# Performance work log

Hardware: AMD Instinct MI355X
Metric: run time of the kernel (lower is better)

Reference implementation:

```python
import jax, jax.numpy as jnp
import numpy as np
from jax import lax

MAX_C = 16       # MAX_MERGE_NUMS
COND_THRES = 0.2
IOU_THRES = 0.3
CLASS_OFFSET = 1e4  # shift per-class so cross-class BEV IoU == 0 (emulates per-class loop)


def setup_inputs() -> dict:
    key = jax.random.key(0)
    k1, k2, k3, k4, k5 = jax.random.split(key, 5)
    B, N = 4, 4096
    # realistic 3D boxes: centers, positive sizes, heading
    centers = jax.random.normal(k1, (B, N, 3), jnp.float32) * 20.0
    sizes = jax.random.uniform(k2, (B, N, 3), jnp.float32, 0.5, 4.5)
    heading = jax.random.uniform(k3, (B, N, 1), jnp.float32, -np.pi, np.pi)
    boxes = jnp.concatenate([centers, sizes, heading], -1)  # [B,N,7]
    scores = jax.random.uniform(k4, (B, N), jnp.float32)
    labels = jax.random.randint(k5, (B, N), 0, 3, jnp.int32)
    kw = jax.random.split(jax.random.fold_in(key, 1), 2)
    W1 = jax.random.normal(kw[0], (7, 64), jnp.float32) * 0.3
    b1 = jnp.zeros((64,), jnp.float32)
    W2 = jax.random.normal(kw[1], (64, 1), jnp.float32) * 0.3
    b2 = jnp.zeros((1,), jnp.float32)
    return {"boxes": boxes, "scores": scores, "labels": labels,
            "W1": W1, "b1": b1, "W2": W2, "b2": b2}


def _nms_merge_frame(boxes, scores, labels, W1, b1, W2, b2):
    # boxes [N,7], scores [N], labels [N] int32
    N = boxes.shape[0]
    valid = scores > COND_THRES                       # cond_mask
    skey = jnp.where(valid, scores, -jnp.inf)
    order = jnp.argsort(-skey)                        # score descending
    boxes, scores = boxes[order], scores[order]
    labels, valid = labels[order], valid[order]

    # nearest-BEV (axis-aligned) IoU; class offset keeps classes disjoint
    off = labels.astype(boxes.dtype) * CLASS_OFFSET
    cx, cy = boxes[:, 0] + off, boxes[:, 1]
    hx, hy = boxes[:, 3] * 0.5, boxes[:, 4] * 0.5
    x1, x2, y1, y2 = cx - hx, cx + hx, cy - hy, cy + hy
    ix = jnp.clip(jnp.minimum(x2[:, None], x2[None]) - jnp.maximum(x1[:, None], x1[None]), 0.0)
    iy = jnp.clip(jnp.minimum(y2[:, None], y2[None]) - jnp.maximum(y1[:, None], y1[None]), 0.0)
    inter = ix * iy                                   # [N,N]
    area = (x2 - x1) * (y2 - y1)
    iou = inter / jnp.clip(area[:, None] + area[None] - inter, 1e-6)
    overlap = iou > IOU_THRES                         # includes self

    # greedy clustering: highest-score remaining box leads its cluster
    def body(i, st):
        alive, cid = st
        lead = alive[i]
        take = alive & overlap[i] & lead
        cid = jnp.where(take, i, cid)
        return alive & (~take), cid
    alive, cid = lax.fori_loop(0, N, body,
                               (valid, jnp.full((N,), -1, jnp.int32)))
    leader = cid == jnp.arange(N, dtype=jnp.int32)    # cluster representatives

    # rank of each box within its cluster (score order preserved)
    idx = jnp.arange(N)
    same = (cid[None, :] == cid[:, None]) & (cid[:, None] >= 0)
    rank = (same & (idx[None, :] < idx[:, None])).sum(-1)  # [N]

    # scatter up to MAX_C members per cluster (zero-padded buffers)
    dest = jnp.where((cid >= 0) & (rank < MAX_C), cid, N)  # N = dump row
    clusters = jnp.zeros((N + 1, MAX_C, 7), boxes.dtype)
    clusters = clusters.at[dest, jnp.minimum(rank, MAX_C - 1)].set(boxes)[:N]

    # merge network: per-box MLP -> softmax weights over cluster slots
    h = jax.nn.relu(clusters @ W1 + b1)               # [N,MAX_C,64]
    logits = (h @ W2 + b2)[..., 0]                    # [N,MAX_C]
    slot_ok = jnp.any(clusters != 0, -1)
    logits = jnp.where(slot_ok, logits, -1e9)
    w = jax.nn.softmax(logits, -1)
    merged = jnp.einsum('nc,ncd->nd', w, clusters)    # [N,7]

    # masked scatter: non-positive merged sizes fall back to leader sizes
    size = jnp.where(merged[:, 3:6] <= 0, boxes[:, 3:6], merged[:, 3:6])
    out_box = jnp.concatenate([merged[:, :3], size, merged[:, 6:7]], -1)
    info = jnp.concatenate([out_box, scores[:, None],
                            labels.astype(boxes.dtype)[:, None]], -1)  # [N,9]
    info = jnp.where(leader[:, None], info, 0.0)
    return info, leader


def reference(boxes, scores, labels, W1, b1, W2, b2):
    info, leader = jax.vmap(_nms_merge_frame,
                            in_axes=(0, 0, 0, None, None, None, None))(
        boxes, scores, labels, W1, b1, W2, b2)
    return info, leader
```

## Files before the change

kernel.cpp:

```cpp
#include <hip/hip_runtime.h>
#include <stdint.h>

#pragma clang fp contract(off)

#define BF 4
#define NN 4096
#define MAXC 16
#define PL 2048
#define WL 32
#define WF 24
#define TRI_CAP (64 * (WL * (WL + 1) / 2))

typedef unsigned long long u64;
typedef uint32_t u32;

__device__ __forceinline__ u64 shfl64(u64 v, int src) {
  return (u64)__shfl((long long)v, src, 64);
}
__device__ __forceinline__ u64 readlane64(u64 v, int l) {
  u32 lo = (u32)__builtin_amdgcn_readlane((int)(u32)v, l);
  u32 hi = (u32)__builtin_amdgcn_readlane((int)(u32)(v >> 32), l);
  return ((u64)hi << 32) | lo;
}
__device__ __forceinline__ u64 greedy64_iso(u64 D, u64 rem, u64 onlyme) {
  u64 lead = 0;
  while (rem) {
    u64 t = D & rem;
    u64 iso = __ballot(t == onlyme) & rem;
    lead |= iso;
    rem &= ~iso;
    if (!rem) break;
    int b = __builtin_ctzll(rem);
    lead |= 1ull << b;
    rem &= ~readlane64(D, b);
    if (!rem) break;
    b = __builtin_ctzll(rem);
    lead |= 1ull << b;
    rem &= ~readlane64(D, b);
  }
  return lead;
}

__global__ __launch_bounds__(1024) void sort_kernel(
    const float* __restrict__ scores, u64* __restrict__ keyS)
{
  __shared__ u64 keyA[NN];
  __shared__ u64 keyB[NN];
  __shared__ int cnt16[16][65];
  __shared__ int waveTot[16];
  __shared__ int waveBase[16];
  const int f = blockIdx.x, tid = threadIdx.x;
  const int wave = tid >> 6, lane = tid & 63;
  const u64 ltmask = (1ull << lane) - 1ull;

  for (int s = 0; s < 4; s++) {
    int idx = tid + 1024 * s;
    float sc = scores[f * NN + idx];
    bool valid = sc > 0.2f;
    u32 bits = __float_as_uint(sc);
    u32 m = bits ^ ((bits >> 31) ? 0xFFFFFFFFu : 0x80000000u);
    u32 hi = valid ? ~m : 0xFFFFFFFFu;
    keyA[idx] = ((u64)hi << 32) | (u32)idx;
  }
  __syncthreads();

  u64* src = keyA;
  u64* dst = keyB;
  for (int pass = 0; pass < 7; pass++) {
    const int shift = 32 + 4 * pass;
    u64 kreg[4]; int dreg[4], rreg[4];
    for (int s = 0; s < 4; s++) {
      const int c = wave * 4 + s;
      u64 k = src[c * 64 + lane];
      int d = (int)((k >> shift) & 15);
      u64 B0 = __ballot((d & 1) != 0);
      u64 B1 = __ballot((d & 2) != 0);
      u64 B2 = __ballot((d & 4) != 0);
      u64 B3 = __ballot((d & 8) != 0);
      u64 M = ((d & 1) ? B0 : ~B0) & ((d & 2) ? B1 : ~B1)
            & ((d & 4) ? B2 : ~B2) & ((d & 8) ? B3 : ~B3);
      rreg[s] = __popcll(M & ltmask);
      int bin = lane & 15;
      u64 Mb = ((bin & 1) ? B0 : ~B0) & ((bin & 2) ? B1 : ~B1)
             & ((bin & 4) ? B2 : ~B2) & ((bin & 8) ? B3 : ~B3);
      if (lane < 16) cnt16[bin][c] = __popcll(Mb);
      kreg[s] = k; dreg[s] = d;
    }
    __syncthreads();
    {
      int v = cnt16[wave][lane];
      int incl = v;
      for (int off2 = 1; off2 < 64; off2 <<= 1) {
        int up = __shfl_up(incl, off2, 64);
        if (lane >= off2) incl += up;
      }
      if (lane == 63) waveTot[wave] = incl;
      __syncthreads();
      if (wave == 0) {
        int tv = (lane < 16) ? waveTot[lane] : 0;
        int ts = tv;
        for (int off2 = 1; off2 < 16; off2 <<= 1) {
          int up = __shfl_up(ts, off2, 64);
          if (lane >= off2) ts += up;
        }
        if (lane < 16) waveBase[lane] = ts - tv;
      }
      __syncthreads();
      cnt16[wave][lane] = waveBase[wave] + incl - v;
    }
    __syncthreads();
    for (int s = 0; s < 4; s++) {
      const int c = wave * 4 + s;
      int pos = cnt16[dreg[s]][c] + rreg[s];
      dst[pos] = kreg[s];
    }
    __syncthreads();
    u64* tmp = src; src = dst; dst = tmp;
  }
  for (int s = 0; s < 4; s++) {
    int p = tid + 1024 * s;
    keyS[f * NN + p] = src[p];
  }
}

__global__ __launch_bounds__(256) void countscan_kernel(
    const u64* __restrict__ keyS, const int* __restrict__ labels,
    int* __restrict__ chunkOffG, int* __restrict__ VbufL)
{
  __shared__ int cnt[64][3];
  const int f = blockIdx.x, tid = threadIdx.x;
  const int wave = tid >> 6, lane = tid & 63;
  for (int s = 0; s < 16; s++) {
    int chunk = wave * 16 + s;
    int p = chunk * 64 + lane;
    u64 kv = keyS[f * NN + p];
    bool valid = (u32)(kv >> 32) != 0xFFFFFFFFu;
    int g = (int)(kv & 0xFFFFFFFFull);
    int l = valid ? labels[f * NN + g] : 3;
    u64 B0 = __ballot((l & 1) != 0);
    u64 B1 = __ballot((l & 2) != 0);
    if (lane < 3) {
      u64 Mb = ((lane & 1) ? B0 : ~B0) & ((lane & 2) ? B1 : ~B1);
      cnt[chunk][lane] = __popcll(Mb);
    }
  }
  __syncthreads();
  if (wave == 0) {
    for (int ll = 0; ll < 3; ll++) {
      int v = cnt[lane][ll];
      int incl = v;
      for (int off2 = 1; off2 < 64; off2 <<= 1) {
        int up = __shfl_up(incl, off2, 64);
        if (lane >= off2) incl += up;
      }
      chunkOffG[(f * 64 + lane) * 3 + ll] = incl - v;
      if (lane == 63) VbufL[f * 3 + ll] = incl;
    }
  }
}

__global__ __launch_bounds__(256) void gather_kernel(
    const u64* __restrict__ keyS, const float* __restrict__ boxes,
    const float* __restrict__ scores, const int* __restrict__ labels,
    const int* __restrict__ chunkOffG,
    float* __restrict__ sboxes, float* __restrict__ sscore, float* __restrict__ slabel,
    int* __restrict__ lab_slot, int* __restrict__ loc_slot,
    int* __restrict__ pglob,
    float* __restrict__ px1, float* __restrict__ px2, float* __restrict__ py1,
    float* __restrict__ py2, float* __restrict__ parea)
{
  const int gs = blockIdx.x * 256 + threadIdx.x;
  const int f = gs >> 12, p = gs & (NN - 1);
  const int lane = threadIdx.x & 63, chunk = p >> 6;
  const u64 ltmask = (1ull << lane) - 1ull;
  u64 kv = keyS[gs];
  bool valid = (u32)(kv >> 32) != 0xFFFFFFFFu;
  int g = (int)(kv & 0xFFFFFFFFull);
  const float* bp = boxes + (size_t)(f * NN + g) * 7;
  float b0 = bp[0], b1v = bp[1], b2v = bp[2], b3 = bp[3], b4 = bp[4], b5 = bp[5], b6 = bp[6];
  int lab = labels[f * NN + g];
  const int o = f * NN + p;
  float* sb = sboxes + (size_t)o * 7;
  sb[0] = b0; sb[1] = b1v; sb[2] = b2v; sb[3] = b3; sb[4] = b4; sb[5] = b5; sb[6] = b6;
  sscore[o] = scores[f * NN + g];
  slabel[o] = (float)lab;
  int l = valid ? lab : 3;
  u64 B0 = __ballot((l & 1) != 0);
  u64 B1 = __ballot((l & 2) != 0);
  u64 M = ((l & 1) ? B0 : ~B0) & ((l & 2) ? B1 : ~B1);
  int rank = __popcll(M & ltmask);
  if (l < 3) {
    int loc = chunkOffG[(f * 64 + chunk) * 3 + l] + rank;
    int pi = (f * 3 + l) * PL + loc;
    float off = (float)l * 10000.0f;
    float cx = b0 + off, cy = b1v;
    float hx = b3 * 0.5f, hy = b4 * 0.5f;
    float x1 = cx - hx, x2 = cx + hx, y1 = cy - hy, y2 = cy + hy;
    float area = (x2 - x1) * (y2 - y1);
    pglob[pi] = p;
    px1[pi] = x1; px2[pi] = x2; py1[pi] = y1; py2[pi] = y2; parea[pi] = area;
    lab_slot[o] = l; loc_slot[o] = loc;
  } else {
    lab_slot[o] = -1; loc_slot[o] = -1;
  }
}

__global__ __launch_bounds__(256) void mask_kernel(
    const float* __restrict__ px1, const float* __restrict__ px2,
    const float* __restrict__ py1, const float* __restrict__ py2,
    const float* __restrict__ parea, const int* __restrict__ pglob,
    const int* __restrict__ VbufL,
    u64* __restrict__ maskP, u64* __restrict__ triT)
{
  __shared__ float4 cbox[1024];
  __shared__ float carea[1024];
  const int bx = blockIdx.x;
  const int fl = bx >> 8, rem = bx & 255;
  const int rt = rem >> 1, wt = rem & 1;
  const int r0 = rt * 16;
  const int Vl = VbufL[fl];
  if (r0 >= Vl) return;
  if (wt * 1024 >= Vl) return;
  const int tid = threadIdx.x;
  for (int q = tid; q < 1024; q += 256) {
    int c = fl * PL + wt * 1024 + q;
    cbox[q] = make_float4(px1[c], px2[c], py1[c], py2[c]);
    carea[q] = parea[c];
  }
  __syncthreads();
  const int row = r0 + (tid & 15);
  const int wl = tid >> 4;
  const int cw = wt * 16 + wl;
  const int nc = Vl - cw * 64;
  if (row >= Vl || nc <= 0) return;
  const int rg = fl * PL + row;
  const float rx1 = px1[rg], rx2 = px2[rg], ry1 = py1[rg], ry2 = py2[rg], ra = parea[rg];
  u64 bits = 0;
  const int qb = wl * 64;
  for (int b = 0; b < 64; b++) {
    float4 cb = cbox[qb + b];
    float ca = carea[qb + b];
    float ix = fminf(rx2, cb.y) - fmaxf(rx1, cb.x);
    ix = fmaxf(ix, 0.0f);
    float iy = fminf(ry2, cb.w) - fmaxf(ry1, cb.z);
    iy = fmaxf(iy, 0.0f);
    float inter = ix * iy;
    float den = fmaxf((ra + ca) - inter, 1e-6f);
    float iou = inter / den;
    bits |= ((u64)(iou > 0.3f)) << b;
  }
  if (nc < 64) bits &= (1ull << nc) - 1ull;
  const int f = fl / 3;
  const int p = pglob[fl * PL + row];
  maskP[((size_t)f * NN + p) * WL + cw] = bits;
  if (row >= 64 * cw) {
    const int W = (Vl + 63) >> 6;
    int base = 64 * (cw * W - (cw * (cw - 1)) / 2);
    triT[(size_t)fl * TRI_CAP + base + (row - 64 * cw)] = bits;
  }
}

__global__ __launch_bounds__(64) void nms_kernel(
    const u64* __restrict__ triT, const int* __restrict__ VbufL,
    u64* __restrict__ leadersP)
{
  __shared__ u64 tri[64 * (WF * (WF + 1) / 2) + 128];
  const int fl = blockIdx.x, lane = threadIdx.x;
  const int Vl = VbufL[fl];
  const int W = (Vl + 63) >> 6;
  const u64* mT = triT + (size_t)fl * TRI_CAP;
  const u64 onlyme = 1ull << lane;
  u64 alive = 0;
  if (lane < WL) {
    int rb = Vl - 64 * lane;
    alive = (rb >= 64) ? ~0ull : ((rb > 0) ? ((1ull << rb) - 1ull) : 0ull);
  }
  u64 myLead = 0;

  if (W > 0 && W <= WF) {
    const int totw = 64 * (W * (W + 1) / 2);
    const int nch = (totw * 8 + 1023) >> 10;
    const char* g = (const char*)mT;
    char* l = (char*)tri;
    int batch = 0;
    for (int it = 0; it < nch; it++) {
      __builtin_amdgcn_global_load_lds(
          (const __attribute__((address_space(1))) unsigned int*)(g + (size_t)it * 1024 + (size_t)lane * 16),
          (__attribute__((address_space(3))) unsigned int*)(l + (size_t)it * 1024),
          16, 0, 0);
      if (++batch == 48) {
        asm volatile("s_waitcnt vmcnt(0)" ::: "memory");
        batch = 0;
      }
    }
    asm volatile("s_waitcnt vmcnt(0)" ::: "memory");
    int offw = 0;
    u64 D = tri[lane];
    for (int w = 0; w < W; w++) {
      const int offw_next = offw + 64 * (W - w);
      u64 Dnext = (w + 1 < W) ? tri[offw_next + lane] : 0;
      u64 lead = greedy64_iso(D, readlane64(alive, w), onlyme);
      if (lane == w) myLead = lead;
      if (lead) {
        const u64* strm = tri + offw;
        int v = w + 1;
        for (; v + 3 < W; v += 4) {
          u64 a0 = strm[64 * (v - w) + lane];
          u64 a1 = strm[64 * (v + 1 - w) + lane];
          u64 a2 = strm[64 * (v + 2 - w) + lane];
          u64 a3 = strm[64 * (v + 3 - w) + lane];
          u64 c0 = __ballot((a0 & lead) != 0ull);
          u64 c1 = __ballot((a1 & lead) != 0ull);
          u64 c2 = __ballot((a2 & lead) != 0ull);
          u64 c3 = __ballot((a3 & lead) != 0ull);
          if (lane == v)     alive &= ~c0;
          if (lane == v + 1) alive &= ~c1;
          if (lane == v + 2) alive &= ~c2;
          if (lane == v + 3) alive &= ~c3;
        }
        for (; v < W; v++) {
          u64 a0 = strm[64 * (v - w) + lane];
          u64 c0 = __ballot((a0 & lead) != 0ull);
          if (lane == v) alive &= ~c0;
        }
      }
      D = Dnext;
      offw = offw_next;
    }
  } else if (W > 0) {
    int offw = 0;
    for (int w = 0; w < W; w++) {
      const u64* strm = mT + offw;
      u64 D = strm[lane];
      u64 lead = greedy64_iso(D, readlane64(alive, w), onlyme);
      if (lane == w) myLead = lead;
      if (lead) {
        for (int v = w + 1; v < W; v++) {
          u64 a0 = strm[64 * (v - w) + lane];
          u64 c0 = __ballot((a0 & lead) != 0ull);
          if (lane == v) alive &= ~c0;
        }
      }
      offw += 64 * (W - w);
    }
  }
  if (lane < WL) leadersP[fl * WL + lane] = myLead;
}

__global__ __launch_bounds__(256) void cid_kernel(
    const u64* __restrict__ maskP, const u64* __restrict__ leadersP,
    const int* __restrict__ lab_slot, const int* __restrict__ loc_slot,
    const int* __restrict__ VbufL, int* __restrict__ cidP)
{
  const int g = blockIdx.x * 4 + (threadIdx.x >> 6);
  const int lane = threadIdx.x & 63;
  const int f = g >> 12, p = g & (NN - 1);
  const int l = lab_slot[f * NN + p];
  if (l < 0) return;
  const int fl = f * 3 + l;
  const int loc = loc_slot[f * NN + p];
  const int Wl = (VbufL[fl] + 63) >> 6;
  u64 L = 0, m = 0;
  if (lane < Wl) {
    L = leadersP[fl * WL + lane];
    m = maskP[((size_t)f * NN + p) * WL + lane];
  }
  const int g6 = loc >> 6, b6 = loc & 63;
  u64 pmask = (lane < g6) ? ~0ull
            : (lane == g6 ? ((b6 == 63) ? ~0ull : ((1ull << (b6 + 1)) - 1ull)) : 0ull);
  u64 v = m & L & pmask;
  u64 bl = __ballot(v != 0ull);
  int cid = -1;
  if (bl != 0ull) {
    int w = __builtin_ctzll(bl);
    u64 vw = shfl64(v, w);
    cid = w * 64 + __builtin_ctzll(vw);
  }
  if (lane == 0) cidP[fl * PL + loc] = cid;
}

__global__ __launch_bounds__(64) void mm_kernel(
    const u64* __restrict__ maskP, const u64* __restrict__ leadersP,
    const int* __restrict__ cidP, const int* __restrict__ lab_slot,
    const int* __restrict__ loc_slot, const int* __restrict__ pglob,
    const int* __restrict__ VbufL,
    const float* __restrict__ sboxes, const float* __restrict__ sscore,
    const float* __restrict__ slabel,
    const float* __restrict__ W1, const float* __restrict__ b1,
    const float* __restrict__ W2, const float* __restrict__ b2,
    float* __restrict__ out)
{
  const int bi = blockIdx.x;
  const int f = bi >> 12, i = bi & (NN - 1);
  const int lane = threadIdx.x;
  const int o = f * NN + i;
  float* info = out + (size_t)o * 9;
  float* lead = out + (size_t)BF * NN * 9 + o;
  const int l = lab_slot[o];
  bool isLead = false;
  int loc = 0, fl = 0;
  if (l >= 0) {
    fl = f * 3 + l;
    loc = loc_slot[o];
    isLead = (leadersP[fl * WL + (loc >> 6)] >> (loc & 63)) & 1ull;
  }
  if (!isLead) {
    if (lane < 9) info[lane] = 0.0f;
    if (lane == 0) *lead = 0.0f;
    return;
  }
  __shared__ int mlist[MAXC];
  __shared__ float mb[MAXC][7];
  __shared__ float lg[MAXC];
  __shared__ float wn[MAXC];
  const u64* mrow = maskP + (size_t)o * WL;
  const int Wl = (VbufL[fl] + 63) >> 6;
  int total = 0;
  for (int w = loc >> 6; w < Wl && total < MAXC; w++) {
    u64 word = mrow[w];
    int pos = w * 64 + lane;
    bool cand = ((word >> lane) & 1ull) && (cidP[fl * PL + pos] == loc);
    u64 mbal = __ballot(cand);
    int r = __popcll(mbal & ((1ull << lane) - 1ull));
    int slot = total + r;
    if (cand && slot < MAXC) mlist[slot] = pglob[fl * PL + pos];
    total += __popcll(mbal);
  }
  const int cnt = min(total, MAXC);
  __syncthreads();
  if (lane < cnt) {
    int j = mlist[lane];
    const float* bp = sboxes + (size_t)(f * NN + j) * 7;
    for (int d = 0; d < 7; d++) mb[lane][d] = bp[d];
  }
  float w1r[7];
  for (int d = 0; d < 7; d++) w1r[d] = W1[d * 64 + lane];
  const float b1c = b1[lane], w2c = W2[lane], b2v = b2[0];
  __syncthreads();
  for (int s = 0; s < cnt; s++) {
    float t = b1c;
    for (int d = 0; d < 7; d++) t += mb[s][d] * w1r[d];
    float h = fmaxf(t, 0.0f);
    float v = h * w2c;
    for (int off2 = 32; off2 > 0; off2 >>= 1) v += __shfl_xor(v, off2, 64);
    if (lane == 0) lg[s] = v + b2v;
  }
  __syncthreads();
  float mx = -1e30f;
  for (int s = 0; s < cnt; s++) mx = fmaxf(mx, lg[s]);
  float den = 0.0f;
  for (int s = 0; s < cnt; s++) den += expf(lg[s] - mx);
  if (lane < cnt) wn[lane] = expf(lg[lane] - mx) / den;
  __syncthreads();
  float val = 0.0f;
  if (lane < 7) {
    float acc = 0.0f;
    for (int s = 0; s < cnt; s++) acc += wn[s] * mb[s][lane];
    val = acc;
    if (lane >= 3 && lane <= 5 && val <= 0.0f) val = sboxes[(size_t)o * 7 + lane];
  } else if (lane == 7) {
    val = sscore[o];
  } else if (lane == 8) {
    val = slabel[o];
  }
  if (lane < 9) info[lane] = val;
  if (lane == 0) *lead = 1.0f;
}

extern "C" void kernel_launch(void* const* d_in, const int* in_sizes, int n_in,
                              void* d_out, int out_size, void* d_ws, size_t ws_size,
                              hipStream_t stream)
{
  const float* boxes  = (const float*)d_in[0];
  const float* scores = (const float*)d_in[1];
  const int*   labels = (const int*)d_in[2];
  const float* W1     = (const float*)d_in[3];
  const float* b1     = (const float*)d_in[4];
  const float* W2     = (const float*)d_in[5];
  const float* b2     = (const float*)d_in[6];
  float* out = (float*)d_out;

  char* ws = (char*)d_ws;
  size_t off = 0;
  auto alloc = [&](size_t bytes) -> void* {
    void* p = ws + off;
    off = (off + bytes + 255) & ~(size_t)255;
    return p;
  };
  u64*   keyS    = (u64*)  alloc((size_t)BF * NN * 8);
  int*   chunkOffG=(int*)  alloc((size_t)BF * 64 * 3 * 4);
  float* sboxes  = (float*)alloc((size_t)BF * NN * 7 * 4);
  float* sscore  = (float*)alloc((size_t)BF * NN * 4);
  float* slabel  = (float*)alloc((size_t)BF * NN * 4);
  int*   lab_slot= (int*)  alloc((size_t)BF * NN * 4);
  int*   loc_slot= (int*)  alloc((size_t)BF * NN * 4);
  int*   pglob   = (int*)  alloc((size_t)BF * 3 * PL * 4);
  float* px1     = (float*)alloc((size_t)BF * 3 * PL * 4);
  float* px2     = (float*)alloc((size_t)BF * 3 * PL * 4);
  float* py1     = (float*)alloc((size_t)BF * 3 * PL * 4);
  float* py2     = (float*)alloc((size_t)BF * 3 * PL * 4);
  float* parea   = (float*)alloc((size_t)BF * 3 * PL * 4);
  int*   VbufL   = (int*)  alloc((size_t)BF * 3 * 4);
  u64*   leadersP= (u64*)  alloc((size_t)BF * 3 * WL * 8);
  int*   cidP    = (int*)  alloc((size_t)BF * 3 * PL * 4);
  u64*   maskP   = (u64*)  alloc((size_t)BF * NN * WL * 8);
  u64*   triT    = (u64*)  alloc((size_t)BF * 3 * TRI_CAP * 8);
  (void)  alloc(32768);

  sort_kernel<<<BF, 1024, 0, stream>>>(scores, keyS);
  countscan_kernel<<<BF, 256, 0, stream>>>(keyS, labels, chunkOffG, VbufL);
  gather_kernel<<<BF * NN / 256, 256, 0, stream>>>(keyS, boxes, scores, labels,
                                                   chunkOffG, sboxes, sscore,
                                                   slabel, lab_slot, loc_slot,
                                                   pglob, px1, px2, py1, py2,
                                                   parea);
  mask_kernel<<<BF * 3 * 256, 256, 0, stream>>>(px1, px2, py1, py2, parea,
                                                pglob, VbufL, maskP, triT);
  nms_kernel<<<BF * 3, 64, 0, stream>>>(triT, VbufL, leadersP);
  cid_kernel<<<BF * NN / 4, 256, 0, stream>>>(maskP, leadersP, lab_slot,
                                              loc_slot, VbufL, cidP);
  mm_kernel<<<BF * NN, 64, 0, stream>>>(maskP, leadersP, cidP, lab_slot,
                                        loc_slot, pglob, VbufL, sboxes,
                                        sscore, slabel, W1, b1, W2, b2, out);
}
```

Baseline: 165.6 us.

## Replace single-block radix sort with parallel rank sort; pack four merge waves per block

New measurement: 159.6 us. -3.6%, faster.

```diff
diff --git a/kernel.cpp b/kernel.cpp
--- a/kernel.cpp
+++ b/kernel.cpp
@@ -13,6 +13,8 @@
 
 typedef unsigned long long u64;
 typedef uint32_t u32;
+
+#define WAVE_SYNC() asm volatile("s_waitcnt lgkmcnt(0)" ::: "memory")
 
 __device__ __forceinline__ u64 shfl64(u64 v, int src) {
   return (u64)__shfl((long long)v, src, 64);
@@ -41,85 +43,35 @@
   return lead;
 }
 
-__global__ __launch_bounds__(1024) void sort_kernel(
+__global__ __launch_bounds__(256) void rank_kernel(
     const float* __restrict__ scores, u64* __restrict__ keyS)
 {
-  __shared__ u64 keyA[NN];
-  __shared__ u64 keyB[NN];
-  __shared__ int cnt16[16][65];
-  __shared__ int waveTot[16];
-  __shared__ int waveBase[16];
-  const int f = blockIdx.x, tid = threadIdx.x;
-  const int wave = tid >> 6, lane = tid & 63;
-  const u64 ltmask = (1ull << lane) - 1ull;
-
-  for (int s = 0; s < 4; s++) {
-    int idx = tid + 1024 * s;
+  __shared__ u64 keys[NN];
+  __shared__ int cnt[4][64];
+  const int f = blockIdx.x >> 6, rb = blockIdx.x & 63;
+  const int tid = threadIdx.x, wave = tid >> 6, lane = tid & 63;
+  for (int s = 0; s < 16; s++) {
+    int idx = tid + 256 * s;
     float sc = scores[f * NN + idx];
     bool valid = sc > 0.2f;
     u32 bits = __float_as_uint(sc);
     u32 m = bits ^ ((bits >> 31) ? 0xFFFFFFFFu : 0x80000000u);
     u32 hi = valid ? ~m : 0xFFFFFFFFu;
-    keyA[idx] = ((u64)hi << 32) | (u32)idx;
+    keys[idx] = ((u64)hi << 32) | (u32)idx;
   }
   __syncthreads();
-
-  u64* src = keyA;
-  u64* dst = keyB;
-  for (int pass = 0; pass < 7; pass++) {
-    const int shift = 32 + 4 * pass;
-    u64 kreg[4]; int dreg[4], rreg[4];
-    for (int s = 0; s < 4; s++) {
-      const int c = wave * 4 + s;
-      u64 k = src[c * 64 + lane];
-      int d = (int)((k >> shift) & 15);
-      u64 B0 = __ballot((d & 1) != 0);
-      u64 B1 = __ballot((d & 2) != 0);
-      u64 B2 = __ballot((d & 4) != 0);
-      u64 B3 = __ballot((d & 8) != 0);
-      u64 M = ((d & 1) ? B0 : ~B0) & ((d & 2) ? B1 : ~B1)
-            & ((d & 4) ? B2 : ~B2) & ((d & 8) ? B3 : ~B3);
-      rreg[s] = __popcll(M & ltmask);
-      int bin = lane & 15;
-      u64 Mb = ((bin & 1) ? B0 : ~B0) & ((bin & 2) ? B1 : ~B1)
-             & ((bin & 4) ? B2 : ~B2) & ((bin & 8) ? B3 : ~B3);
-      if (lane < 16) cnt16[bin][c] = __popcll(Mb);
-      kreg[s] = k; dreg[s] = d;
-    }
-    __syncthreads();
-    {
-      int v = cnt16[wave][lane];
-      int incl = v;
-      for (int off2 = 1; off2 < 64; off2 <<= 1) {
-        int up = __shfl_up(incl, off2, 64);
-        if (lane >= off2) incl += up;
-      }
-      if (lane == 63) waveTot[wave] = incl;
-      __syncthreads();
-      if (wave == 0) {
-        int tv = (lane < 16) ? waveTot[lane] : 0;
-        int ts = tv;
-        for (int off2 = 1; off2 < 16; off2 <<= 1) {
-          int up = __shfl_up(ts, off2, 64);
-          if (lane >= off2) ts += up;
-        }
-        if (lane < 16) waveBase[lane] = ts - tv;
-      }
-      __syncthreads();
-      cnt16[wave][lane] = waveBase[wave] + incl - v;
-    }
-    __syncthreads();
-    for (int s = 0; s < 4; s++) {
-      const int c = wave * 4 + s;
-      int pos = cnt16[dreg[s]][c] + rreg[s];
-      dst[pos] = kreg[s];
-    }
-    __syncthreads();
-    u64* tmp = src; src = dst; dst = tmp;
-  }
-  for (int s = 0; s < 4; s++) {
-    int p = tid + 1024 * s;
-    keyS[f * NN + p] = src[p];
+  const int row = rb * 64 + lane;
+  const u64 mykey = keys[row];
+  int c = 0;
+  const int j0 = wave * 1024;
+#pragma unroll 8
+  for (int j = j0; j < j0 + 1024; j++)
+    c += (keys[j] < mykey) ? 1 : 0;
+  cnt[wave][lane] = c;
+  __syncthreads();
+  if (wave == 0) {
+    int rank = cnt[0][lane] + cnt[1][lane] + cnt[2][lane] + cnt[3][lane];
+    keyS[f * NN + rank] = mykey;
   }
 }
 
@@ -379,7 +331,7 @@
   if (lane == 0) cidP[fl * PL + loc] = cid;
 }
 
-__global__ __launch_bounds__(64) void mm_kernel(
+__global__ __launch_bounds__(256) void mm_kernel(
     const u64* __restrict__ maskP, const u64* __restrict__ leadersP,
     const int* __restrict__ cidP, const int* __restrict__ lab_slot,
     const int* __restrict__ loc_slot, const int* __restrict__ pglob,
@@ -390,9 +342,13 @@
     const float* __restrict__ W2, const float* __restrict__ b2,
     float* __restrict__ out)
 {
-  const int bi = blockIdx.x;
+  __shared__ int   mlistS[4][MAXC];
+  __shared__ float mbS[4][MAXC][7];
+  __shared__ float lgS[4][MAXC];
+  __shared__ float wnS[4][MAXC];
+  const int wv = threadIdx.x >> 6, lane = threadIdx.x & 63;
+  const int bi = blockIdx.x * 4 + wv;
   const int f = bi >> 12, i = bi & (NN - 1);
-  const int lane = threadIdx.x;
   const int o = f * NN + i;
   float* info = out + (size_t)o * 9;
   float* lead = out + (size_t)BF * NN * 9 + o;
@@ -409,10 +365,10 @@
     if (lane == 0) *lead = 0.0f;
     return;
   }
-  __shared__ int mlist[MAXC];
-  __shared__ float mb[MAXC][7];
-  __shared__ float lg[MAXC];
-  __shared__ float wn[MAXC];
+  int* mlist = mlistS[wv];
+  float (*mb)[7] = mbS[wv];
+  float* lg = lgS[wv];
+  float* wn = wnS[wv];
   const u64* mrow = maskP + (size_t)o * WL;
   const int Wl = (VbufL[fl] + 63) >> 6;
   int total = 0;
@@ -427,7 +383,7 @@
     total += __popcll(mbal);
   }
   const int cnt = min(total, MAXC);
-  __syncthreads();
+  WAVE_SYNC();
   if (lane < cnt) {
     int j = mlist[lane];
     const float* bp = sboxes + (size_t)(f * NN + j) * 7;
@@ -436,7 +392,7 @@
   float w1r[7];
   for (int d = 0; d < 7; d++) w1r[d] = W1[d * 64 + lane];
   const float b1c = b1[lane], w2c = W2[lane], b2v = b2[0];
-  __syncthreads();
+  WAVE_SYNC();
   for (int s = 0; s < cnt; s++) {
     float t = b1c;
     for (int d = 0; d < 7; d++) t += mb[s][d] * w1r[d];
@@ -445,13 +401,13 @@
     for (int off2 = 32; off2 > 0; off2 >>= 1) v += __shfl_xor(v, off2, 64);
     if (lane == 0) lg[s] = v + b2v;
   }
-  __syncthreads();
+  WAVE_SYNC();
   float mx = -1e30f;
   for (int s = 0; s < cnt; s++) mx = fmaxf(mx, lg[s]);
   float den = 0.0f;
   for (int s = 0; s < cnt; s++) den += expf(lg[s] - mx);
   if (lane < cnt) wn[lane] = expf(lg[lane] - mx) / den;
-  __syncthreads();
+  WAVE_SYNC();
   float val = 0.0f;
   if (lane < 7) {
     float acc = 0.0f;
@@ -507,7 +463,7 @@
   u64*   triT    = (u64*)  alloc((size_t)BF * 3 * TRI_CAP * 8);
   (void)  alloc(32768);
 
-  sort_kernel<<<BF, 1024, 0, stream>>>(scores, keyS);
+  rank_kernel<<<BF * 64, 256, 0, stream>>>(scores, keyS);
   countscan_kernel<<<BF, 256, 0, stream>>>(keyS, labels, chunkOffG, VbufL);
   gather_kernel<<<BF * NN / 256, 256, 0, stream>>>(keyS, boxes, scores, labels,
                                                    chunkOffG, sboxes, sscore,
@@ -519,7 +475,7 @@
   nms_kernel<<<BF * 3, 64, 0, stream>>>(triT, VbufL, leadersP);
   cid_kernel<<<BF * NN / 4, 256, 0, stream>>>(maskP, leadersP, lab_slot,
                                               loc_slot, VbufL, cidP);
-  mm_kernel<<<BF * NN, 64, 0, stream>>>(maskP, leadersP, cidP, lab_slot,
-                                        loc_slot, pglob, VbufL, sboxes,
-                                        sscore, slabel, W1, b1, W2, b2, out);
-}
+  mm_kernel<<<BF * NN / 4, 256, 0, stream>>>(maskP, leadersP, cidP, lab_slot,
+                                             loc_slot, pglob, VbufL, sboxes,
+                                             sscore, slabel, W1, b1, W2, b2, out);
+}
```
